# Optimization experiments

Hardware: AMD Instinct MI355X
Metric: run time of the kernel (lower is better)

Reference implementation:

```python
import jax, jax.numpy as jnp
import numpy as np

XBITS = 8  # bitconfig['xbits']


def quantize(x, bits=XBITS):
    """Per-tensor dynamic fixed-point fake-quant.
    topk(|x|, k=len, largest=False).max() == max(|x|), so the 'percentile' is a no-op.
    scale = 2**(bits - ceil(log2(max|x|)) - 1); clamp(round(x*scale), -t, t)/scale.
    """
    thresh = float(2 ** (bits - 1) - 1)
    max_abs = jnp.max(jnp.abs(x))
    # get_scale returns 0 on log2 domain error (threshold <= 0)
    exp = jnp.where(max_abs > 0, jnp.ceil(jnp.log2(max_abs)), jnp.zeros((), x.dtype))
    scale = jnp.exp2(jnp.asarray(bits, x.dtype) - exp - 1)
    return jnp.clip(jnp.round(x * scale), -thresh, thresh) / scale


def setup_inputs() -> dict:
    key = jax.random.key(0)
    k1, k2, k3 = jax.random.split(key, 3)
    N, D_in, D_out = 65536, 1024, 1024
    x = jax.random.normal(k1, (N, D_in), dtype=jnp.float32)
    weight = jax.random.normal(k2, (D_out, D_in), dtype=jnp.float32) * (1.0 / np.sqrt(D_in))
    bias = jax.random.normal(k3, (D_out,), dtype=jnp.float32) * (1.0 / np.sqrt(D_in))
    return {"x": x, "weight": weight, "bias": bias}


def reference(x, weight, bias):
    # FixedLinearFunction.forward: quantize both operands, matmul; bias is NOT added.
    q_x = quantize(x)
    q_w = quantize(weight)
    return q_x @ q_w.T  # [N, D_out]
```

## Files before the change

kernel.cpp:

```cpp
#include <hip/hip_runtime.h>
#include <stdint.h>

typedef int v4i  __attribute__((ext_vector_type(4)));
typedef int v16i __attribute__((ext_vector_type(16)));

__device__ __forceinline__ void async_load16(const void* g, void* l) {
    auto gp = (const __attribute__((address_space(1))) unsigned int*)(uintptr_t)g;
    auto lp = (__attribute__((address_space(3))) unsigned int*)(unsigned int)(uintptr_t)l;
    __builtin_amdgcn_global_load_lds(gp, lp, 16, 0, 0);
}

__global__ void k_init(unsigned* bits) {
    if (threadIdx.x < 2) bits[threadIdx.x] = 0u;
}

__global__ void k_absmax2(const float4* __restrict__ x, int nx4,
                          const float4* __restrict__ w, int nw4,
                          unsigned* __restrict__ bits) {
    const int XB = 2048;
    const float4* in; int n4, b, nb; unsigned* ob;
    if (blockIdx.x < XB) { in = x; n4 = nx4; b = blockIdx.x;      nb = XB;              ob = bits;     }
    else                 { in = w; n4 = nw4; b = blockIdx.x - XB; nb = gridDim.x - XB;  ob = bits + 1; }
    float m = 0.0f;
    int stride = nb * blockDim.x;
    for (int i = b * blockDim.x + threadIdx.x; i < n4; i += stride) {
        float4 v = in[i];
        m = fmaxf(m, fmaxf(fmaxf(fabsf(v.x), fabsf(v.y)),
                           fmaxf(fabsf(v.z), fabsf(v.w))));
    }
    #pragma unroll
    for (int off = 32; off > 0; off >>= 1)
        m = fmaxf(m, __shfl_down(m, off, 64));
    __shared__ float red[4];
    int lane = threadIdx.x & 63, wv = threadIdx.x >> 6;
    if (lane == 0) red[wv] = m;
    __syncthreads();
    if (threadIdx.x == 0) {
        m = fmaxf(fmaxf(red[0], red[1]), fmaxf(red[2], red[3]));
        atomicMax(ob, __float_as_uint(m));
    }
}

__global__ void k_scales(const unsigned* __restrict__ bits, float* __restrict__ sc) {
    float s[2];
    for (int i = 0; i < 2; ++i) {
        float m = __uint_as_float(bits[i]);
        int ex = 0;
        if (m > 0.0f) {
            int e;
            float f = frexpf(m, &e);
            ex = (f == 0.5f) ? (e - 1) : e;
        }
        s[i] = ldexpf(1.0f, 7 - ex);
    }
    sc[0] = s[0];
    sc[1] = s[1];
    sc[2] = 1.0f / (s[0] * s[1]);
}

__global__ void k_quant2(const float4* __restrict__ x, int* __restrict__ qx, int nx4,
                         const float4* __restrict__ w, int* __restrict__ qw, int nw4,
                         const float* __restrict__ scp) {
    const int XB = 4096;
    const float4* in; int* out; int n4, b, nb; float s;
    if (blockIdx.x < XB) { in = x; out = qx; n4 = nx4; b = blockIdx.x;      nb = XB;             s = scp[0]; }
    else                 { in = w; out = qw; n4 = nw4; b = blockIdx.x - XB; nb = gridDim.x - XB; s = scp[1]; }
    int stride = nb * blockDim.x;
    for (int i = b * blockDim.x + threadIdx.x; i < n4; i += stride) {
        float4 v = in[i];
        int qa = (int)rintf(v.x * s); qa = qa > 127 ? 127 : (qa < -127 ? -127 : qa);
        int qb = (int)rintf(v.y * s); qb = qb > 127 ? 127 : (qb < -127 ? -127 : qb);
        int qc = (int)rintf(v.z * s); qc = qc > 127 ? 127 : (qc < -127 ? -127 : qc);
        int qd = (int)rintf(v.w * s); qd = qd > 127 ? 127 : (qd < -127 ? -127 : qd);
        out[i] = (qa & 0xff) | ((qb & 0xff) << 8) | ((qc & 0xff) << 16) | (qd << 24);
    }
}

#define GBAR()  __builtin_amdgcn_s_barrier()
#define WAITV4() asm volatile("s_waitcnt vmcnt(4)" ::: "memory")
#define WAITV0() asm volatile("s_waitcnt vmcnt(0)" ::: "memory")

__global__ __launch_bounds__(512, 2) void k_gemm(const signed char* __restrict__ A,
                                                 const signed char* __restrict__ B,
                                                 float* __restrict__ out,
                                                 const float* __restrict__ scp) {
    __shared__ __align__(16) signed char lds[4 * 16384];
    const int tid  = threadIdx.x;
    const int lane = tid & 63;
    const int wave = tid >> 6;
    const int wm   = wave >> 2;
    const int wn   = wave & 3;
    const int l31  = lane & 31;
    const int lhi  = lane >> 5;

    const int orig = blockIdx.x;
    const int v    = (orig & 7) * 128 + (orig >> 3);
    const int n0   = (v & 3) * 256;
    const int m0   = (v >> 2) * 256;

    v16i acc[4][2];
    #pragma unroll
    for (int a = 0; a < 4; ++a)
        #pragma unroll
        for (int b = 0; b < 2; ++b)
            #pragma unroll
            for (int i = 0; i < 16; ++i) acc[a][b][i] = 0;

    const signed char* gA[2];
    const signed char* gB[2];
    #pragma unroll
    for (int s = 0; s < 2; ++s) {
        int i = s * 512 + tid;
        int p = i >> 2;
        int q = (i & 3) ^ ((p >> 1) & 3);
        gA[s] = A + (size_t)(m0 + p) * 1024 + q * 16;
        gB[s] = B + (size_t)(n0 + p) * 1024 + q * 16;
    }

    auto STAGE = [&](int cur, int k0) {
        signed char* base = lds + cur * 32768;
        #pragma unroll
        for (int s = 0; s < 2; ++s) {
            async_load16(gA[s] + k0, base +         s * 8192 + tid * 16);
            async_load16(gB[s] + k0, base + 16384 + s * 8192 + tid * 16);
        }
    };

    const int key = (l31 >> 1) & 3;
    auto COMPUTE = [&](int cur) {
        const signed char* Ab = lds + cur * 32768;
        const signed char* Bb = Ab + 16384;
        #pragma unroll
        for (int ks = 0; ks < 2; ++ks) {
            const int slot = ((ks * 2 + lhi) ^ key) * 16;
            v4i af[4], bf[2];
            #pragma unroll
            for (int tm = 0; tm < 4; ++tm)
                af[tm] = *(const v4i*)(Ab + (wm * 128 + tm * 32 + l31) * 64 + slot);
            #pragma unroll
            for (int tn = 0; tn < 2; ++tn)
                bf[tn] = *(const v4i*)(Bb + (wn * 64 + tn * 32 + l31) * 64 + slot);
            #pragma unroll
            for (int tm = 0; tm < 4; ++tm)
                #pragma unroll
                for (int tn = 0; tn < 2; ++tn)
                    acc[tm][tn] = __builtin_amdgcn_mfma_i32_32x32x32_i8(
                        af[tm], bf[tn], acc[tm][tn], 0, 0, 0);
        }
    };

    STAGE(0, 0);
    STAGE(1, 64);

    #pragma unroll 2
    for (int t = 0; t < 14; ++t) {
        WAITV4();
        GBAR();
        COMPUTE(t & 1);
        GBAR();
        STAGE(t & 1, (t + 2) * 64);
    }
    WAITV4(); GBAR(); COMPUTE(0); GBAR();
    WAITV0(); GBAR(); COMPUTE(1);

    const float inv = scp[0];
    #pragma unroll
    for (int tm = 0; tm < 4; ++tm)
        #pragma unroll
        for (int tn = 0; tn < 2; ++tn)
            #pragma unroll
            for (int r = 0; r < 16; ++r) {
                int row = m0 + wm * 128 + tm * 32 + (r & 3) + 8 * (r >> 2) + 4 * lhi;
                int col = n0 + wn * 64 + tn * 32 + l31;
                out[(size_t)row * 1024 + col] = (float)acc[tm][tn][r] * inv;
            }
}

extern "C" void kernel_launch(void* const* d_in, const int* in_sizes, int n_in,
                              void* d_out, int out_size, void* d_ws, size_t ws_size,
                              hipStream_t stream) {
    const float* x = (const float*)d_in[0];
    const float* w = (const float*)d_in[1];
    float* out = (float*)d_out;

    const int NX = 65536 * 1024;
    const int NW = 1024 * 1024;

    char* ws = (char*)d_ws;
    unsigned* bits = (unsigned*)ws;
    float* sc = (float*)(ws + 8);
    signed char* qx = (signed char*)(ws + 256);
    signed char* qw = qx + (size_t)NX;

    k_init<<<1, 64, 0, stream>>>(bits);
    k_absmax2<<<2048 + 128, 256, 0, stream>>>((const float4*)x, NX / 4,
                                              (const float4*)w, NW / 4, bits);
    k_scales<<<1, 1, 0, stream>>>(bits, sc);
    k_quant2<<<4096 + 128, 256, 0, stream>>>((const float4*)x, (int*)qx, NX / 4,
                                             (const float4*)w, (int*)qw, NW / 4, sc);

    k_gemm<<<dim3(1024), 512, 0, stream>>>(qx, qw, out, sc + 2);
}
```

Baseline: 587.8 us.

## Triple-buffer GEMM LDS and interleave async loads with MFMA

The int8 GEMM moves from two LDS buffers to three rotating ones. This removes the second barrier per k-step, because the buffer being filled is never the one being read. Each global-to-LDS load piece is now issued between MFMA groups inside the compute loop, and the MFMA groups run at raised wave priority through s_setprio. The aim is to overlap memory traffic with matrix math and cut synchronisation stalls. The cost is 96 KB of LDS per block, which likely prevents two blocks from sharing a CU and lowers occupancy.

```diff
diff --git a/kernel.cpp b/kernel.cpp
--- a/kernel.cpp
+++ b/kernel.cpp
@@ -79,12 +79,13 @@
 #define GBAR()  __builtin_amdgcn_s_barrier()
 #define WAITV4() asm volatile("s_waitcnt vmcnt(4)" ::: "memory")
 #define WAITV0() asm volatile("s_waitcnt vmcnt(0)" ::: "memory")
+#define CFENCE() asm volatile("" ::: "memory")
 
 __global__ __launch_bounds__(512, 2) void k_gemm(const signed char* __restrict__ A,
                                                  const signed char* __restrict__ B,
                                                  float* __restrict__ out,
                                                  const float* __restrict__ scp) {
-    __shared__ __align__(16) signed char lds[4 * 16384];
+    __shared__ __align__(16) signed char lds[3 * 32768];
     const int tid  = threadIdx.x;
     const int lane = tid & 63;
     const int wave = tid >> 6;
@@ -117,51 +118,56 @@
         gB[s] = B + (size_t)(n0 + p) * 1024 + q * 16;
     }
 
-    auto STAGE = [&](int cur, int k0) {
-        signed char* base = lds + cur * 32768;
-        #pragma unroll
-        for (int s = 0; s < 2; ++s) {
-            async_load16(gA[s] + k0, base +         s * 8192 + tid * 16);
-            async_load16(gB[s] + k0, base + 16384 + s * 8192 + tid * 16);
-        }
+    auto STAGE_PIECE = [&](signed char* base, int k0, int j) {
+        int s = j >> 1;
+        if ((j & 1) == 0) async_load16(gA[s] + k0, base +         s * 8192 + tid * 16);
+        else              async_load16(gB[s] + k0, base + 16384 + s * 8192 + tid * 16);
     };
 
+    {
+        signed char* b0 = lds;
+        signed char* b1 = lds + 32768;
+        #pragma unroll
+        for (int j = 0; j < 4; ++j) STAGE_PIECE(b0, 0, j);
+        #pragma unroll
+        for (int j = 0; j < 4; ++j) STAGE_PIECE(b1, 64, j);
+    }
+
     const int key = (l31 >> 1) & 3;
-    auto COMPUTE = [&](int cur) {
-        const signed char* Ab = lds + cur * 32768;
-        const signed char* Bb = Ab + 16384;
+
+    signed char* rd  = lds;
+    signed char* mid = lds + 32768;
+    signed char* st  = lds + 65536;
+
+    #pragma unroll
+    for (int t = 0; t < 16; ++t) {
+        if (t == 15) { WAITV0(); } else { WAITV4(); }
+        GBAR();
+        CFENCE();
+        const signed char* Ab = rd;
+        const signed char* Bb = rd + 16384;
+        const int k2 = (t + 2) * 64;
+        const bool dostage = (t < 14);
         #pragma unroll
         for (int ks = 0; ks < 2; ++ks) {
             const int slot = ((ks * 2 + lhi) ^ key) * 16;
-            v4i af[4], bf[2];
+            v4i bf0 = *(const v4i*)(Bb + (wn * 64 +      l31) * 64 + slot);
+            v4i bf1 = *(const v4i*)(Bb + (wn * 64 + 32 + l31) * 64 + slot);
             #pragma unroll
-            for (int tm = 0; tm < 4; ++tm)
-                af[tm] = *(const v4i*)(Ab + (wm * 128 + tm * 32 + l31) * 64 + slot);
-            #pragma unroll
-            for (int tn = 0; tn < 2; ++tn)
-                bf[tn] = *(const v4i*)(Bb + (wn * 64 + tn * 32 + l31) * 64 + slot);
-            #pragma unroll
-            for (int tm = 0; tm < 4; ++tm)
-                #pragma unroll
-                for (int tn = 0; tn < 2; ++tn)
-                    acc[tm][tn] = __builtin_amdgcn_mfma_i32_32x32x32_i8(
-                        af[tm], bf[tn], acc[tm][tn], 0, 0, 0);
+            for (int h = 0; h < 2; ++h) {
+                v4i a0 = *(const v4i*)(Ab + (wm * 128 + (h * 2    ) * 32 + l31) * 64 + slot);
+                v4i a1 = *(const v4i*)(Ab + (wm * 128 + (h * 2 + 1) * 32 + l31) * 64 + slot);
+                if (dostage) STAGE_PIECE(st, k2, ks * 2 + h);
+                __builtin_amdgcn_s_setprio(1);
+                acc[h*2  ][0] = __builtin_amdgcn_mfma_i32_32x32x32_i8(a0, bf0, acc[h*2  ][0], 0, 0, 0);
+                acc[h*2  ][1] = __builtin_amdgcn_mfma_i32_32x32x32_i8(a0, bf1, acc[h*2  ][1], 0, 0, 0);
+                acc[h*2+1][0] = __builtin_amdgcn_mfma_i32_32x32x32_i8(a1, bf0, acc[h*2+1][0], 0, 0, 0);
+                acc[h*2+1][1] = __builtin_amdgcn_mfma_i32_32x32x32_i8(a1, bf1, acc[h*2+1][1], 0, 0, 0);
+                __builtin_amdgcn_s_setprio(0);
+            }
         }
-    };
-
-    STAGE(0, 0);
-    STAGE(1, 64);
-
-    #pragma unroll 2
-    for (int t = 0; t < 14; ++t) {
-        WAITV4();
-        GBAR();
-        COMPUTE(t & 1);
-        GBAR();
-        STAGE(t & 1, (t + 2) * 64);
-    }
-    WAITV4(); GBAR(); COMPUTE(0); GBAR();
-    WAITV0(); GBAR(); COMPUTE(1);
+        signed char* tmp = rd; rd = mid; mid = st; st = tmp;
+    }
 
     const float inv = scp[0];
     #pragma unroll
```

Result: faster. 574.4 us (-2.3%).
